# Kernel tuning notes

Measured on AMD Instinct MI355X. Metric: run time of the kernel, lower is better.

The kernel has to match this reference:

```python
import jax, jax.numpy as jnp
import numpy as np

VOCAB, D, M = 400000, 50, 128
B, L = 64, 512

def setup_inputs() -> dict:
    key = jax.random.key(0)
    k1, k2, k3, k4, k5, k6 = jax.random.split(key, 6)
    return {
        "x": jax.random.randint(k1, (B, L), 0, VOCAB),
        "amp_table": jax.random.normal(k2, (VOCAB, D), dtype=jnp.float32),
        "pha_table": jax.random.uniform(k3, (VOCAB, D), dtype=jnp.float32) * (2.0 * np.pi),
        "mix_table": jax.random.normal(k4, (VOCAB, 1), dtype=jnp.float32),
        "kernel_real": jax.random.normal(k5, (M, D), dtype=jnp.float32),
        "kernel_imag": jax.random.normal(k6, (M, D), dtype=jnp.float32),
    }

def reference(x, amp_table, pha_table, mix_table, kernel_real, kernel_imag):
    # Embedding lookups: amplitude, phase, and mixture logit per token
    amp = amp_table[x]            # [B, L, D]
    pha = pha_table[x]            # [B, L, D]
    mix = mix_table[x][..., 0]    # [B, L]

    # softmax over sequence dim (dim=1) -> per-token mixture weights
    w = jax.nn.softmax(mix, axis=1)  # [B, L]

    # complex token vector v = amp * exp(i * pha)
    vr = amp * jnp.cos(pha)       # [B, L, D]
    vi = amp * jnp.sin(pha)       # [B, L, D]

    # Fused density + mixture: rho = sum_l w_l * v_l v_l^H  (never materialize [B,L,D,D])
    rho_r = jnp.einsum('bl,bld,ble->bde', w, vr, vr) + jnp.einsum('bl,bld,ble->bde', w, vi, vi)
    rho_i = jnp.einsum('bl,bld,ble->bde', w, vi, vr) - jnp.einsum('bl,bld,ble->bde', w, vr, vi)

    # Row-normalized complex measurement vectors m_k
    norm = jnp.sqrt(jnp.sum(kernel_real**2 + kernel_imag**2, axis=-1, keepdims=True))
    kr = kernel_real / norm       # [M, D]
    ki = kernel_imag / norm       # [M, D]

    # p_k = Re(m_k^H rho m_k); conj(m)_d m_e = (kr_d kr_e + ki_d ki_e) + i(kr_d ki_e - ki_d kr_e)
    p = (jnp.einsum('bde,md,me->bm', rho_r, kr, kr)
         + jnp.einsum('bde,md,me->bm', rho_r, ki, ki)
         - jnp.einsum('bde,md,me->bm', rho_i, kr, ki)
         + jnp.einsum('bde,md,me->bm', rho_i, ki, kr))
    return p                      # [B, M]
```

## Files before the change

### kernel.cpp

```cpp
#include <hip/hip_runtime.h>
#include <math.h>

#define VOCAB 400000
#define D     50
#define DP    56
#define ROWQ  14
#define NQH   7
#define MM    128
#define LL    512
#define BB    64
#define NCHUNK 16
#define CHUNK 32
#define TPR   8
#define ROUNDS (CHUNK / TPR)
#define ITEMS (TPR * DP)
#define NTHREADS 256

__global__ void __launch_bounds__(1024) zero_kernel(float* __restrict__ out) {
    out[blockIdx.x * 1024 + threadIdx.x] = 0.0f;
}

__global__ void __launch_bounds__(NTHREADS)
qdnn_main(const int*   __restrict__ x,
          const float* __restrict__ amp_table,
          const float* __restrict__ pha_table,
          const float* __restrict__ mix_table,
          const float* __restrict__ kernel_real,
          const float* __restrict__ kernel_imag,
          float* __restrict__ out)
{
    __shared__ int    s_x[LL];
    __shared__ float  s_w[LL];
    __shared__ float  s_red[8];
    __shared__ float4 s_vr4[2][TPR * ROWQ];
    __shared__ float4 s_vi4[2][TPR * ROWQ];

    const int tid   = threadIdx.x;
    const int b     = blockIdx.x >> 4;
    const int chunk = blockIdx.x & (NCHUNK - 1);
    const int wave  = tid >> 6;
    const int lane  = tid & 63;
    const int half  = lane >> 5;
    const int m     = wave * 32 + (lane & 31);

    const int* xg = x + b * LL;
    s_x[tid]       = xg[tid];
    s_x[tid + 256] = xg[tid + 256];
    __syncthreads();

    float v0 = mix_table[s_x[tid]];
    float v1 = mix_table[s_x[tid + 256]];
    float lmax = fmaxf(v0, v1);
    #pragma unroll
    for (int off = 32; off > 0; off >>= 1)
        lmax = fmaxf(lmax, __shfl_down(lmax, off));
    if (lane == 0) s_red[wave] = lmax;
    __syncthreads();
    const float bmax = fmaxf(fmaxf(s_red[0], s_red[1]), fmaxf(s_red[2], s_red[3]));
    const float e0 = __expf(v0 - bmax);
    const float e1 = __expf(v1 - bmax);
    s_w[tid]       = e0;
    s_w[tid + 256] = e1;
    float esum = e0 + e1;
    #pragma unroll
    for (int off = 32; off > 0; off >>= 1)
        esum += __shfl_down(esum, off);
    if (lane == 0) s_red[4 + wave] = esum;
    __syncthreads();
    const float inv = 1.0f / (s_red[4] + s_red[5] + s_red[6] + s_red[7]);
    s_w[tid]       *= inv;
    s_w[tid + 256] *= inv;

    float4 krg[NQH], kig[NQH];
    #pragma unroll
    for (int q = 0; q < NQH; ++q) {
        const int dbase = half * 28 + q * 4;
        float4 a, c;
        a.x = (dbase + 0 < D) ? kernel_real[m * D + dbase + 0] : 0.0f;
        a.y = (dbase + 1 < D) ? kernel_real[m * D + dbase + 1] : 0.0f;
        a.z = (dbase + 2 < D) ? kernel_real[m * D + dbase + 2] : 0.0f;
        a.w = (dbase + 3 < D) ? kernel_real[m * D + dbase + 3] : 0.0f;
        c.x = (dbase + 0 < D) ? kernel_imag[m * D + dbase + 0] : 0.0f;
        c.y = (dbase + 1 < D) ? kernel_imag[m * D + dbase + 1] : 0.0f;
        c.z = (dbase + 2 < D) ? kernel_imag[m * D + dbase + 2] : 0.0f;
        c.w = (dbase + 3 < D) ? kernel_imag[m * D + dbase + 3] : 0.0f;
        krg[q] = a; kig[q] = c;
    }

    float s2p = 0.0f;
    #pragma unroll
    for (int q = 0; q < NQH; ++q) {
        const float4 a = krg[q], c = kig[q];
        s2p = fmaf(a.x, a.x, fmaf(c.x, c.x, s2p));
        s2p = fmaf(a.y, a.y, fmaf(c.y, c.y, s2p));
        s2p = fmaf(a.z, a.z, fmaf(c.z, c.z, s2p));
        s2p = fmaf(a.w, a.w, fmaf(c.w, c.w, s2p));
    }
    s2p += __shfl_xor(s2p, 32);
    const float s2 = 1.0f / s2p;

    const int  j0 = tid,        tok0 = j0 / DP, d0 = j0 - tok0 * DP;
    const int  j1 = tid + 256,  tok1 = j1 / DP, d1 = j1 - tok1 * DP;
    const bool p0v  = (d0 < D);
    const bool has1 = (j1 < ITEMS);
    const bool p1v  = has1 && (d1 < D);
    const int  lbase = chunk * CHUNK;

    {
        float a0 = 0.f, q0 = 0.f, a1 = 0.f, q1 = 0.f;
        if (p0v) { int idx = s_x[lbase + tok0]; a0 = amp_table[idx * D + d0]; q0 = pha_table[idx * D + d0]; }
        if (p1v) { int idx = s_x[lbase + tok1]; a1 = amp_table[idx * D + d1]; q1 = pha_table[idx * D + d1]; }
        float* vr = (float*)s_vr4[0];
        float* vi = (float*)s_vi4[0];
        float sn, cs;
        __sincosf(q0, &sn, &cs);
        vr[j0] = p0v ? a0 * cs : 0.0f;
        vi[j0] = p0v ? a0 * sn : 0.0f;
        if (has1) {
            __sincosf(q1, &sn, &cs);
            vr[j1] = p1v ? a1 * cs : 0.0f;
            vi[j1] = p1v ? a1 * sn : 0.0f;
        }
    }
    __syncthreads();

    float pacc = 0.0f;
    for (int r = 0; r < ROUNDS; ++r) {
        const int cur = r & 1;

        float a0 = 0.f, q0 = 0.f, a1 = 0.f, q1 = 0.f;
        if (r < ROUNDS - 1) {
            const int lb = lbase + (r + 1) * TPR;
            if (p0v) { int idx = s_x[lb + tok0]; a0 = amp_table[idx * D + d0]; q0 = pha_table[idx * D + d0]; }
            if (p1v) { int idx = s_x[lb + tok1]; a1 = amp_table[idx * D + d1]; q1 = pha_table[idx * D + d1]; }
        }

        const float* wrow = s_w + lbase + r * TPR;
        #pragma unroll
        for (int t = 0; t < TPR; ++t) {
            const float4* vr4 = s_vr4[cur] + t * ROWQ + half * NQH;
            const float4* vi4 = s_vi4[cur] + t * ROWQ + half * NQH;
            float Ar0 = 0.f, Ar1 = 0.f, Ai0 = 0.f, Ai1 = 0.f;
            #pragma unroll
            for (int q = 0; q < NQH; ++q) {
                const float4 rv = vr4[q], iv = vi4[q];
                const float4 kr = krg[q], ki = kig[q];
                Ar0 = fmaf(kr.x, rv.x, Ar0); Ar0 = fmaf(ki.x, iv.x, Ar0);
                Ai0 = fmaf(kr.x, iv.x, Ai0); Ai0 = fmaf(-ki.x, rv.x, Ai0);
                Ar1 = fmaf(kr.y, rv.y, Ar1); Ar1 = fmaf(ki.y, iv.y, Ar1);
                Ai1 = fmaf(kr.y, iv.y, Ai1); Ai1 = fmaf(-ki.y, rv.y, Ai1);
                Ar0 = fmaf(kr.z, rv.z, Ar0); Ar0 = fmaf(ki.z, iv.z, Ar0);
                Ai0 = fmaf(kr.z, iv.z, Ai0); Ai0 = fmaf(-ki.z, rv.z, Ai0);
                Ar1 = fmaf(kr.w, rv.w, Ar1); Ar1 = fmaf(ki.w, iv.w, Ar1);
                Ai1 = fmaf(kr.w, iv.w, Ai1); Ai1 = fmaf(-ki.w, rv.w, Ai1);
            }
            float Ar = Ar0 + Ar1, Ai = Ai0 + Ai1;
            Ar += __shfl_xor(Ar, 32);
            Ai += __shfl_xor(Ai, 32);
            pacc = fmaf(wrow[t], fmaf(Ar, Ar, Ai * Ai), pacc);
        }

        if (r < ROUNDS - 1) {
            const int nxt = cur ^ 1;
            float* vr = (float*)s_vr4[nxt];
            float* vi = (float*)s_vi4[nxt];
            float sn, cs;
            __sincosf(q0, &sn, &cs);
            vr[j0] = p0v ? a0 * cs : 0.0f;
            vi[j0] = p0v ? a0 * sn : 0.0f;
            if (has1) {
                __sincosf(q1, &sn, &cs);
                vr[j1] = p1v ? a1 * cs : 0.0f;
                vi[j1] = p1v ? a1 * sn : 0.0f;
            }
        }
        __syncthreads();
    }

    if (half == 0) {
        atomicAdd(&out[b * MM + m], pacc * s2);
    }
}

extern "C" void kernel_launch(void* const* d_in, const int* in_sizes, int n_in,
                              void* d_out, int out_size, void* d_ws, size_t ws_size,
                              hipStream_t stream) {
    const int*   xx  = (const int*)d_in[0];
    const float* amp = (const float*)d_in[1];
    const float* pha = (const float*)d_in[2];
    const float* mix = (const float*)d_in[3];
    const float* kr  = (const float*)d_in[4];
    const float* ki  = (const float*)d_in[5];
    float* out = (float*)d_out;

    hipLaunchKernelGGL(zero_kernel, dim3((BB * MM) / 1024), dim3(1024), 0, stream, out);
    hipLaunchKernelGGL(qdnn_main, dim3(BB * NCHUNK), dim3(NTHREADS), 0, stream,
                       xx, amp, pha, mix, kr, ki, out);
}
```

Before: 181.8 us.

## Compute measurement projections with bf16x3 split MFMA using prepacked kernel fragments

Moves the per-token complex projection onto the matrix cores. Each value is split into bf16 hi and lo parts and four MFMAs per product emulate fp32 accuracy. A new prep kernel packs the normalized kernel into MFMA fragment layout in the workspace, computes the row norms and zeroes the output. Token chunks grow to 64 per block, with half as many blocks, and the hi/lo token vectors are staged in LDS. This trades the scalar FMA inner loop for 8 MFMAs per k-step, at some cost in precision and extra LDS traffic.

New measurement: 174.5 us. 1.04x faster.

```diff
diff --git a/kernel.cpp b/kernel.cpp
--- a/kernel.cpp
+++ b/kernel.cpp
@@ -1,23 +1,85 @@
 #include <hip/hip_runtime.h>
 #include <math.h>
 
-#define VOCAB 400000
-#define D     50
-#define DP    56
-#define ROWQ  14
-#define NQH   7
-#define MM    128
-#define LL    512
-#define BB    64
-#define NCHUNK 16
-#define CHUNK 32
-#define TPR   8
-#define ROUNDS (CHUNK / TPR)
-#define ITEMS (TPR * DP)
+#define D      50
+#define MM     128
+#define LL     512
+#define BB     64
+#define KK     128
+#define KS     136
+#define LT     64
+#define NCH    8
 #define NTHREADS 256
 
-__global__ void __launch_bounds__(1024) zero_kernel(float* __restrict__ out) {
-    out[blockIdx.x * 1024 + threadIdx.x] = 0.0f;
+typedef __attribute__((ext_vector_type(8))) short  short8;
+typedef __attribute__((ext_vector_type(4))) float  float4v;
+
+__device__ __forceinline__ void bsplit(float x, short& hi, short& lo) {
+    unsigned u = __float_as_uint(x);
+    unsigned r = u + 0x7FFFu + ((u >> 16) & 1u);
+    hi = (short)(r >> 16);
+    float res = x - __uint_as_float(r & 0xFFFF0000u);
+    unsigned u2 = __float_as_uint(res);
+    unsigned r2 = u2 + 0x7FFFu + ((u2 >> 16) & 1u);
+    lo = (short)(r2 >> 16);
+}
+
+__global__ void __launch_bounds__(NTHREADS)
+qdnn_prep(const float* __restrict__ kernel_real,
+          const float* __restrict__ kernel_imag,
+          float* __restrict__ out,
+          short* __restrict__ ws_frag,
+          float* __restrict__ ws_norm)
+{
+    const int tid = threadIdx.x;
+    if (blockIdx.x == 8) {
+        #pragma unroll
+        for (int j = 0; j < (BB * MM) / NTHREADS; ++j)
+            out[j * NTHREADS + tid] = 0.0f;
+        return;
+    }
+    const int ntile = blockIdx.x;
+    const int lane  = tid & 63;
+    const int kstep = tid >> 6;
+    const int col   = lane & 15;
+    const int g     = lane >> 4;
+    const int m     = ntile * 16 + col;
+    const float* krow = kernel_real + m * D;
+    const float* irow = kernel_imag + m * D;
+
+    short8 fr_hi, fr_lo, fi_hi, fi_lo;
+    float np = 0.0f;
+    #pragma unroll
+    for (int j = 0; j < 8; ++j) {
+        const int k = kstep * 32 + g * 8 + j;
+        float br = 0.0f, bi = 0.0f;
+        if (k < D) {
+            const float a = krow[k], c = irow[k];
+            br = a; bi = -c;
+            np = fmaf(a, a, fmaf(c, c, np));
+        } else if (k < 2 * D) {
+            const float a = krow[k - D], c = irow[k - D];
+            br = c; bi = a;
+        }
+        short h, l;
+        bsplit(br, h, l); fr_hi[j] = h; fr_lo[j] = l;
+        bsplit(bi, h, l); fi_hi[j] = h; fi_lo[j] = l;
+    }
+    const size_t fb = (size_t)((ntile * 4 + kstep) * 4) * 64 * 8;
+    *(short8*)(ws_frag + fb + (size_t)(0 * 64 + lane) * 8) = fr_hi;
+    *(short8*)(ws_frag + fb + (size_t)(1 * 64 + lane) * 8) = fr_lo;
+    *(short8*)(ws_frag + fb + (size_t)(2 * 64 + lane) * 8) = fi_hi;
+    *(short8*)(ws_frag + fb + (size_t)(3 * 64 + lane) * 8) = fi_lo;
+
+    __shared__ float s_nr[NTHREADS];
+    s_nr[tid] = np;
+    __syncthreads();
+    if (tid < 16) {
+        float s = 0.0f;
+        #pragma unroll
+        for (int u = 0; u < 16; ++u) s += s_nr[tid + 16 * u];
+        ws_norm[ntile * 16 + tid] = s;
+    }
 }
 
 __global__ void __launch_bounds__(NTHREADS)
@@ -25,31 +87,29 @@
           const float* __restrict__ amp_table,
           const float* __restrict__ pha_table,
           const float* __restrict__ mix_table,
-          const float* __restrict__ kernel_real,
-          const float* __restrict__ kernel_imag,
+          const short* __restrict__ ws_frag,
+          const float* __restrict__ ws_norm,
           float* __restrict__ out)
 {
-    __shared__ int    s_x[LL];
-    __shared__ float  s_w[LL];
-    __shared__ float  s_red[8];
-    __shared__ float4 s_vr4[2][TPR * ROWQ];
-    __shared__ float4 s_vi4[2][TPR * ROWQ];
-
-    const int tid   = threadIdx.x;
-    const int b     = blockIdx.x >> 4;
-    const int chunk = blockIdx.x & (NCHUNK - 1);
-    const int wave  = tid >> 6;
-    const int lane  = tid & 63;
-    const int half  = lane >> 5;
-    const int m     = wave * 32 + (lane & 31);
+    __shared__ short s_vhi[LT * KS];
+    __shared__ short s_vlo[LT * KS];
+    __shared__ int   s_x[LL];
+    __shared__ float s_w[LL];
+    __shared__ float s_red[8];
+
+    const int tid    = threadIdx.x;
+    const int b      = blockIdx.x >> 3;
+    const int lchunk = blockIdx.x & 7;
+    const int wave   = tid >> 6;
+    const int lane   = tid & 63;
 
     const int* xg = x + b * LL;
     s_x[tid]       = xg[tid];
     s_x[tid + 256] = xg[tid + 256];
     __syncthreads();
 
-    float v0 = mix_table[s_x[tid]];
-    float v1 = mix_table[s_x[tid + 256]];
+    const float v0 = mix_table[s_x[tid]];
+    const float v1 = mix_table[s_x[tid + 256]];
     float lmax = fmaxf(v0, v1);
     #pragma unroll
     for (int off = 32; off > 0; off >>= 1)
@@ -71,114 +131,85 @@
     s_w[tid]       *= inv;
     s_w[tid + 256] *= inv;
 
-    float4 krg[NQH], kig[NQH];
-    #pragma unroll
-    for (int q = 0; q < NQH; ++q) {
-        const int dbase = half * 28 + q * 4;
-        float4 a, c;
-        a.x = (dbase + 0 < D) ? kernel_real[m * D + dbase + 0] : 0.0f;
-        a.y = (dbase + 1 < D) ? kernel_real[m * D + dbase + 1] : 0.0f;
-        a.z = (dbase + 2 < D) ? kernel_real[m * D + dbase + 2] : 0.0f;
-        a.w = (dbase + 3 < D) ? kernel_real[m * D + dbase + 3] : 0.0f;
-        c.x = (dbase + 0 < D) ? kernel_imag[m * D + dbase + 0] : 0.0f;
-        c.y = (dbase + 1 < D) ? kernel_imag[m * D + dbase + 1] : 0.0f;
-        c.z = (dbase + 2 < D) ? kernel_imag[m * D + dbase + 2] : 0.0f;
-        c.w = (dbase + 3 < D) ? kernel_imag[m * D + dbase + 3] : 0.0f;
-        krg[q] = a; kig[q] = c;
-    }
-
-    float s2p = 0.0f;
-    #pragma unroll
-    for (int q = 0; q < NQH; ++q) {
-        const float4 a = krg[q], c = kig[q];
-        s2p = fmaf(a.x, a.x, fmaf(c.x, c.x, s2p));
-        s2p = fmaf(a.y, a.y, fmaf(c.y, c.y, s2p));
-        s2p = fmaf(a.z, a.z, fmaf(c.z, c.z, s2p));
-        s2p = fmaf(a.w, a.w, fmaf(c.w, c.w, s2p));
-    }
-    s2p += __shfl_xor(s2p, 32);
-    const float s2 = 1.0f / s2p;
-
-    const int  j0 = tid,        tok0 = j0 / DP, d0 = j0 - tok0 * DP;
-    const int  j1 = tid + 256,  tok1 = j1 / DP, d1 = j1 - tok1 * DP;
-    const bool p0v  = (d0 < D);
-    const bool has1 = (j1 < ITEMS);
-    const bool p1v  = has1 && (d1 < D);
-    const int  lbase = chunk * CHUNK;
-
     {
-        float a0 = 0.f, q0 = 0.f, a1 = 0.f, q1 = 0.f;
-        if (p0v) { int idx = s_x[lbase + tok0]; a0 = amp_table[idx * D + d0]; q0 = pha_table[idx * D + d0]; }
-        if (p1v) { int idx = s_x[lbase + tok1]; a1 = amp_table[idx * D + d1]; q1 = pha_table[idx * D + d1]; }
-        float* vr = (float*)s_vr4[0];
-        float* vi = (float*)s_vi4[0];
-        float sn, cs;
-        __sincosf(q0, &sn, &cs);
-        vr[j0] = p0v ? a0 * cs : 0.0f;
-        vi[j0] = p0v ? a0 * sn : 0.0f;
-        if (has1) {
-            __sincosf(q1, &sn, &cs);
-            vr[j1] = p1v ? a1 * cs : 0.0f;
-            vi[j1] = p1v ? a1 * sn : 0.0f;
-        }
-    }
-    __syncthreads();
-
-    float pacc = 0.0f;
-    for (int r = 0; r < ROUNDS; ++r) {
-        const int cur = r & 1;
-
-        float a0 = 0.f, q0 = 0.f, a1 = 0.f, q1 = 0.f;
-        if (r < ROUNDS - 1) {
-            const int lb = lbase + (r + 1) * TPR;
-            if (p0v) { int idx = s_x[lb + tok0]; a0 = amp_table[idx * D + d0]; q0 = pha_table[idx * D + d0]; }
-            if (p1v) { int idx = s_x[lb + tok1]; a1 = amp_table[idx * D + d1]; q1 = pha_table[idx * D + d1]; }
-        }
-
-        const float* wrow = s_w + lbase + r * TPR;
-        #pragma unroll
-        for (int t = 0; t < TPR; ++t) {
-            const float4* vr4 = s_vr4[cur] + t * ROWQ + half * NQH;
-            const float4* vi4 = s_vi4[cur] + t * ROWQ + half * NQH;
-            float Ar0 = 0.f, Ar1 = 0.f, Ai0 = 0.f, Ai1 = 0.f;
+        const int tok   = tid >> 2;
+        const int dbase = (tid & 3) * 13;
+        const int gidx  = s_x[lchunk * LT + tok];
+        const float* arow = amp_table + (size_t)gidx * D;
+        const float* prow = pha_table + (size_t)gidx * D;
+        #pragma unroll
+        for (int jj = 0; jj < 13; ++jj) {
+            const int d = dbase + jj;
+            if (d < D) {
+                const float a = arow[d], ph = prow[d];
+                float sn, cs;
+                __sincosf(ph, &sn, &cs);
+                short h, l;
+                bsplit(a * cs, h, l);
+                s_vhi[tok * KS + d] = h;      s_vlo[tok * KS + d] = l;
+                bsplit(a * sn, h, l);
+                s_vhi[tok * KS + D + d] = h;  s_vlo[tok * KS + D + d] = l;
+            }
+        }
+        for (int j = tid; j < LT * (KS - 2 * D); j += NTHREADS) {
+            const int r = j / (KS - 2 * D);
+            const int c = 2 * D + (j - r * (KS - 2 * D));
+            s_vhi[r * KS + c] = 0;
+            s_vlo[r * KS + c] = 0;
+        }
+    }
+    __syncthreads();
+
+    const int l15 = lane & 15;
+    const int g   = lane >> 4;
+    for (int miter = 0; miter < 2; ++miter) {
+        const int ntile = miter * 4 + wave;
+        short8 fr_hi[4], fr_lo[4], fi_hi[4], fi_lo[4];
+        #pragma unroll
+        for (int ks = 0; ks < 4; ++ks) {
+            const size_t fb = (size_t)((ntile * 4 + ks) * 4) * 64 * 8;
+            fr_hi[ks] = *(const short8*)(ws_frag + fb + (size_t)(0 * 64 + lane) * 8);
+            fr_lo[ks] = *(const short8*)(ws_frag + fb + (size_t)(1 * 64 + lane) * 8);
+            fi_hi[ks] = *(const short8*)(ws_frag + fb + (size_t)(2 * 64 + lane) * 8);
+            fi_lo[ks] = *(const short8*)(ws_frag + fb + (size_t)(3 * 64 + lane) * 8);
+        }
+        const float nrm = ws_norm[ntile * 16 + l15];
+
+        float pm = 0.0f;
+        for (int liter = 0; liter < 4; ++liter) {
+            const int lb = liter * 16;
+            float4v ar[4], ai[4];
             #pragma unroll
-            for (int q = 0; q < NQH; ++q) {
-                const float4 rv = vr4[q], iv = vi4[q];
-                const float4 kr = krg[q], ki = kig[q];
-                Ar0 = fmaf(kr.x, rv.x, Ar0); Ar0 = fmaf(ki.x, iv.x, Ar0);
-                Ai0 = fmaf(kr.x, iv.x, Ai0); Ai0 = fmaf(-ki.x, rv.x, Ai0);
-                Ar1 = fmaf(kr.y, rv.y, Ar1); Ar1 = fmaf(ki.y, iv.y, Ar1);
-                Ai1 = fmaf(kr.y, iv.y, Ai1); Ai1 = fmaf(-ki.y, rv.y, Ai1);
-                Ar0 = fmaf(kr.z, rv.z, Ar0); Ar0 = fmaf(ki.z, iv.z, Ar0);
-                Ai0 = fmaf(kr.z, iv.z, Ai0); Ai0 = fmaf(-ki.z, rv.z, Ai0);
-                Ar1 = fmaf(kr.w, rv.w, Ar1); Ar1 = fmaf(ki.w, iv.w, Ar1);
-                Ai1 = fmaf(kr.w, iv.w, Ai1); Ai1 = fmaf(-ki.w, rv.w, Ai1);
-            }
-            float Ar = Ar0 + Ar1, Ai = Ai0 + Ai1;
-            Ar += __shfl_xor(Ar, 32);
-            Ai += __shfl_xor(Ai, 32);
-            pacc = fmaf(wrow[t], fmaf(Ar, Ar, Ai * Ai), pacc);
-        }
-
-        if (r < ROUNDS - 1) {
-            const int nxt = cur ^ 1;
-            float* vr = (float*)s_vr4[nxt];
-            float* vi = (float*)s_vi4[nxt];
-            float sn, cs;
-            __sincosf(q0, &sn, &cs);
-            vr[j0] = p0v ? a0 * cs : 0.0f;
-            vi[j0] = p0v ? a0 * sn : 0.0f;
-            if (has1) {
-                __sincosf(q1, &sn, &cs);
-                vr[j1] = p1v ? a1 * cs : 0.0f;
-                vi[j1] = p1v ? a1 * sn : 0.0f;
-            }
-        }
-        __syncthreads();
-    }
-
-    if (half == 0) {
-        atomicAdd(&out[b * MM + m], pacc * s2);
+            for (int ks = 0; ks < 4; ++ks) {
+                ar[ks] = (float4v)(0.0f);
+                ai[ks] = (float4v)(0.0f);
+            }
+            #pragma unroll
+            for (int ks = 0; ks < 4; ++ks) {
+                const int aoff = (lb + l15) * KS + ks * 32 + g * 8;
+                const short8 ah = *(const short8*)(s_vhi + aoff);
+                const short8 al = *(const short8*)(s_vlo + aoff);
+                ar[ks] = __builtin_amdgcn_mfma_f32_16x16x32_bf16(ah, fr_hi[ks], ar[ks], 0, 0, 0);
+                ar[ks] = __builtin_amdgcn_mfma_f32_16x16x32_bf16(ah, fr_lo[ks], ar[ks], 0, 0, 0);
+                ar[ks] = __builtin_amdgcn_mfma_f32_16x16x32_bf16(al, fr_hi[ks], ar[ks], 0, 0, 0);
+                ar[ks] = __builtin_amdgcn_mfma_f32_16x16x32_bf16(al, fr_lo[ks], ar[ks], 0, 0, 0);
+                ai[ks] = __builtin_amdgcn_mfma_f32_16x16x32_bf16(ah, fi_hi[ks], ai[ks], 0, 0, 0);
+                ai[ks] = __builtin_amdgcn_mfma_f32_16x16x32_bf16(ah, fi_lo[ks], ai[ks], 0, 0, 0);
+                ai[ks] = __builtin_amdgcn_mfma_f32_16x16x32_bf16(al, fi_hi[ks], ai[ks], 0, 0, 0);
+                ai[ks] = __builtin_amdgcn_mfma_f32_16x16x32_bf16(al, fi_lo[ks], ai[ks], 0, 0, 0);
+            }
+            #pragma unroll
+            for (int reg = 0; reg < 4; ++reg) {
+                const float arr = ar[0][reg] + ar[1][reg] + ar[2][reg] + ar[3][reg];
+                const float aii = ai[0][reg] + ai[1][reg] + ai[2][reg] + ai[3][reg];
+                const float wl  = s_w[lchunk * LT + lb + g * 4 + reg];
+                pm = fmaf(wl, fmaf(arr, arr, aii * aii), pm);
+            }
+        }
+        pm += __shfl_xor(pm, 16);
+        pm += __shfl_xor(pm, 32);
+        if (lane < 16)
+            atomicAdd(&out[b * MM + ntile * 16 + l15], pm / nrm);
     }
 }
 
@@ -193,7 +224,11 @@
     const float* ki  = (const float*)d_in[5];
     float* out = (float*)d_out;
 
-    hipLaunchKernelGGL(zero_kernel, dim3((BB * MM) / 1024), dim3(1024), 0, stream, out);
-    hipLaunchKernelGGL(qdnn_main, dim3(BB * NCHUNK), dim3(NTHREADS), 0, stream,
-                       xx, amp, pha, mix, kr, ki, out);
-}
+    short* ws_frag = (short*)d_ws;
+    float* ws_norm = (float*)((char*)d_ws + 131072);
+
+    hipLaunchKernelGGL(qdnn_prep, dim3(9), dim3(NTHREADS), 0, stream,
+                       kr, ki, out, ws_frag, ws_norm);
+    hipLaunchKernelGGL(qdnn_main, dim3(BB * NCH), dim3(NTHREADS), 0, stream,
+                       xx, amp, pha, mix, ws_frag, ws_norm, out);
+}
```
